# Optimization experiments

Hardware: AMD Instinct MI355X
Metric: run time of the kernel (lower is better)

Reference implementation:

```python
import jax, jax.numpy as jnp
import numpy as np

EMBED_DIM = 128
NUM_HEADS = 16
D_K = EMBED_DIM // NUM_HEADS  # must equal n_wires = 8


def setup_inputs() -> dict:
    key = jax.random.key(0)
    k1, k2 = jax.random.split(key)
    x = jax.random.normal(k1, (8, 2048, EMBED_DIM), dtype=jnp.float32)
    theta = jax.random.normal(k2, (D_K,), dtype=jnp.float32)  # trainable RX angles, one per wire
    return {"x": x, "theta": theta}


def _quantum_measure(q, theta):
    # q: [B, H, S, 8]. RX(x)RX(theta) = RX(x+theta); product state gives <Z_i> = cos(phi_i).
    # CNOT chain C(0,1)..C(6,7),C(7,0) in Heisenberg picture:
    #   <Z_0> = prod_{i=1..7} cos(phi_i);  <Z_w> = prod_{i=0..w} cos(phi_i), w>=1.
    c = jnp.cos(q + theta)                       # [B,H,S,8]
    cp = jnp.cumprod(c, axis=-1)                 # prefix products prod_{0..w}
    z0 = jnp.prod(c[..., 1:], axis=-1, keepdims=True)
    return jnp.concatenate([z0, cp[..., 1:]], axis=-1)  # [B,H,S,8]


def reference(x, theta):
    B, S, E = x.shape
    # split heads: [B,S,E] -> [B,H,S,d_k]
    q = x.reshape(B, S, NUM_HEADS, D_K).transpose(0, 2, 1, 3)
    out = _quantum_measure(q, theta)             # [B,H,S,8]
    # merge heads back: [B,S,E]
    out = out.transpose(0, 2, 1, 3).reshape(B, S, E)
    scores = jnp.einsum('bse,bte->bst', out, out) / jnp.sqrt(jnp.float32(D_K))
    attn = jax.nn.softmax(scores, axis=-1)       # dropout = identity in eval mode
    return jnp.einsum('bst,bte->bse', attn, out)
```

## Files before the change

kernel.cpp:

```cpp
#include <hip/hip_runtime.h>

#define NB 8
#define SS 2048
#define DD 128
#define SCALE2 0.5101817664764817f
#define NEGINF -3.0e38f

typedef _Float16 f16x8 __attribute__((ext_vector_type(8)));
typedef float f32x16 __attribute__((ext_vector_type(16)));
typedef unsigned short u16;
typedef u16 u16x8 __attribute__((ext_vector_type(8)));
typedef unsigned int u32;

__device__ __forceinline__ u32 pkrtz(float a, float b) {
    u32 w;
    asm("v_cvt_pkrtz_f16_f32 %0, %1, %2" : "=v"(w) : "v"(a), "v"(b));
    return w;
}

__global__ __launch_bounds__(512) void qmeasure_kernel(const float* __restrict__ x,
                                                       const float* __restrict__ theta,
                                                       u16* __restrict__ G1,
                                                       u16* __restrict__ G2) {
    __shared__ u16 olds[32][136];
    const int bid = blockIdx.x;
    const int b = bid & 7;
    const int t = bid >> 3;
    const int tid = threadIdx.x;
    const int s = tid >> 4;
    const int c = tid & 15;

    float th[8];
    *(float4*)th = *(const float4*)theta;
    *(float4*)(th + 4) = *(const float4*)(theta + 4);

    const float* xp = x + (((size_t)b * SS + t * 32 + s) * DD) + c * 8;
    float4 a = *(const float4*)xp;
    float4 a2 = *(const float4*)(xp + 4);
    float cc[8];
    cc[0] = __cosf(a.x + th[0]);  cc[1] = __cosf(a.y + th[1]);
    cc[2] = __cosf(a.z + th[2]);  cc[3] = __cosf(a.w + th[3]);
    cc[4] = __cosf(a2.x + th[4]); cc[5] = __cosf(a2.y + th[5]);
    cc[6] = __cosf(a2.z + th[6]); cc[7] = __cosf(a2.w + th[7]);
    float o[8];
    o[1] = cc[0] * cc[1];
    o[2] = o[1] * cc[2]; o[3] = o[2] * cc[3]; o[4] = o[3] * cc[4];
    o[5] = o[4] * cc[5]; o[6] = o[5] * cc[6]; o[7] = o[6] * cc[7];
    float z = cc[1] * cc[2]; z *= cc[3]; z *= cc[4]; z *= cc[5]; z *= cc[6]; z *= cc[7];
    o[0] = z;

    u16x8 w;
#pragma unroll
    for (int e = 0; e < 8; ++e) w[e] = __builtin_bit_cast(u16, (_Float16)o[e]);
    *(u16x8*)&olds[s][c * 8] = w;
    __syncthreads();

    {
        const int kc = tid >> 6, hh = (tid >> 5) & 1, r = tid & 31;
        u16x8 g;
#pragma unroll
        for (int u = 0; u < 8; ++u) g[u] = olds[r][kc * 16 + hh * 8 + u];
        *(u16x8*)(G1 + (size_t)b * (SS * DD) + ((size_t)t * 512 + tid) * 8) = g;
    }
    {
        const int lo5 = tid & 31;
        const int hh = (tid >> 5) & 1;
        const int dkc = tid >> 6;
        const int dt = dkc >> 1, kc2 = dkc & 1;
        u16x8 g;
#pragma unroll
        for (int u = 0; u < 8; ++u) g[u] = olds[kc2 * 16 + hh * 8 + u][dt * 32 + lo5];
        const int chunk = t * 512 + dkc * 64 + hh * 32 + lo5;
        *(u16x8*)(G2 + (size_t)b * (SS * DD) + (size_t)chunk * 8) = g;
    }
}

__global__ __launch_bounds__(256, 4) void qattn_kernel(const u16* __restrict__ G1g,
                                                       const u16* __restrict__ G2g,
                                                       float* __restrict__ out) {
    __shared__ float obuf[3][4][16][64];
    __shared__ float mlb[3][2][32];

    const int tid = threadIdx.x;
    const int lane = tid & 63;
    const int kq = tid >> 6;
    const int lo5 = lane & 31;
    const int hi = lane >> 5;
    const int bid = blockIdx.x;
    const int b = bid & 7;
    const int qt = bid >> 3;
    const int lane8 = lane * 8;

    const u16* G1b = G1g + (size_t)b * (SS * DD);
    const u16* G2b = G2g + (size_t)b * (SS * DD);

    f16x8 qf[8];
    {
        const u16* qp = G1b + (size_t)qt * 4096 + lane8;
#pragma unroll
        for (int kc = 0; kc < 8; ++kc) qf[kc] = *(const f16x8*)(qp + kc * 512);
    }

    f32x16 accT[4];
#pragma unroll
    for (int dt = 0; dt < 4; ++dt)
#pragma unroll
        for (int e = 0; e < 16; ++e) accT[dt][e] = 0.f;
    float m = NEGINF, l = 0.f;

    for (int it = 0; it < 16; ++it) {
        const int t = kq * 16 + it;
        const u16* kp = G1b + (size_t)t * 4096 + lane8;
        const u16* vp = G2b + (size_t)t * 4096 + lane8;

        f32x16 acc;
#pragma unroll
        for (int e = 0; e < 16; ++e) acc[e] = 0.f;
        __builtin_amdgcn_s_setprio(1);
#pragma unroll
        for (int kc = 0; kc < 8; ++kc) {
            f16x8 kf = *(const f16x8*)(kp + kc * 512);
            acc = __builtin_amdgcn_mfma_f32_32x32x16_f16(kf, qf[kc], acc, 0, 0, 0);
        }
        __builtin_amdgcn_s_setprio(0);

        float ma = fmaxf(fmaxf(acc[0], acc[1]), acc[2]);
        float mb = fmaxf(fmaxf(acc[8], acc[9]), acc[10]);
        ma = fmaxf(fmaxf(ma, acc[3]), acc[4]);
        mb = fmaxf(fmaxf(mb, acc[11]), acc[12]);
        ma = fmaxf(fmaxf(ma, acc[5]), acc[6]);
        mb = fmaxf(fmaxf(mb, acc[13]), acc[14]);
        ma = fmaxf(fmaxf(ma, acc[7]), mb);
        float tmax = fmaxf(ma, acc[15]) * SCALE2;
        tmax = fmaxf(tmax, __shfl_xor(tmax, 32));
        if (!__all(tmax <= m + 8.f)) {
            const float mnew = fmaxf(m, tmax);
            const float corr = exp2f(m - mnew);
            l *= corr;
#pragma unroll
            for (int dt = 0; dt < 4; ++dt)
#pragma unroll
                for (int e = 0; e < 16; ++e) accT[dt][e] *= corr;
            m = mnew;
        }
#pragma unroll
        for (int r = 0; r < 16; ++r) acc[r] = exp2f(acc[r] * SCALE2 - m);
        float s0 = (acc[0] + acc[1]) + (acc[2] + acc[3]);
        float s1 = (acc[4] + acc[5]) + (acc[6] + acc[7]);
        float s2 = (acc[8] + acc[9]) + (acc[10] + acc[11]);
        float s3 = (acc[12] + acc[13]) + (acc[14] + acc[15]);
        float rowsum = (s0 + s1) + (s2 + s3);
        rowsum += __shfl_xor(rowsum, 32);
        l += rowsum;

        f16x8 pa[2];
#pragma unroll
        for (int kc2 = 0; kc2 < 2; ++kc2) {
            const int r0 = kc2 * 8;
            u32 w0 = pkrtz(acc[r0 + 0], acc[r0 + 1]);
            u32 w2 = pkrtz(acc[r0 + 4], acc[r0 + 5]);
            asm("v_permlane32_swap_b32 %0, %1" : "+v"(w0), "+v"(w2));
            u32 w1 = pkrtz(acc[r0 + 2], acc[r0 + 3]);
            u32 w3 = pkrtz(acc[r0 + 6], acc[r0 + 7]);
            asm("v_permlane32_swap_b32 %0, %1" : "+v"(w1), "+v"(w3));
            union { u32 w[4]; f16x8 v; } u;
            u.w[0] = w0; u.w[1] = w1; u.w[2] = w2; u.w[3] = w3;
            pa[kc2] = u.v;
        }

        __builtin_amdgcn_s_setprio(1);
#pragma unroll
        for (int dt = 0; dt < 4; ++dt) {
            f16x8 vf0 = *(const f16x8*)(vp + (dt * 2 + 0) * 512);
            f16x8 vf1 = *(const f16x8*)(vp + (dt * 2 + 1) * 512);
            f32x16 a = accT[dt];
            a = __builtin_amdgcn_mfma_f32_32x32x16_f16(vf0, pa[0], a, 0, 0, 0);
            a = __builtin_amdgcn_mfma_f32_32x32x16_f16(vf1, pa[1], a, 0, 0, 0);
            accT[dt] = a;
        }
        __builtin_amdgcn_s_setprio(0);
    }

    if (kq > 0) {
        if (hi == 0) {
            mlb[kq - 1][0][lo5] = m;
            mlb[kq - 1][1][lo5] = l;
        }
#pragma unroll
        for (int dt = 0; dt < 4; ++dt)
#pragma unroll
            for (int r = 0; r < 16; ++r)
                obuf[kq - 1][dt][r][lane] = accT[dt][r];
    }
    __syncthreads();
    if (kq == 0) {
        const float mj0 = mlb[0][0][lo5], lj0 = mlb[0][1][lo5];
        const float mj1 = mlb[1][0][lo5], lj1 = mlb[1][1][lo5];
        const float mj2 = mlb[2][0][lo5], lj2 = mlb[2][1][lo5];
        const float ms = fmaxf(fmaxf(m, mj0), fmaxf(mj1, mj2));
        const float w0 = exp2f(m - ms), w1 = exp2f(mj0 - ms);
        const float w2 = exp2f(mj1 - ms), w3 = exp2f(mj2 - ms);
        const float linv = 1.f / (l * w0 + lj0 * w1 + lj1 * w2 + lj2 * w3);
        float* orow = out + ((size_t)b * SS + qt * 32 + lo5) * DD;
#pragma unroll
        for (int dt = 0; dt < 4; ++dt)
#pragma unroll
            for (int r = 0; r < 16; ++r) {
                const float o = accT[dt][r] * w0 + obuf[0][dt][r][lane] * w1 +
                                obuf[1][dt][r][lane] * w2 + obuf[2][dt][r][lane] * w3;
                const int drow = (r & 3) + 8 * (r >> 2) + 4 * hi;
                orow[dt * 32 + drow] = o * linv;
            }
    }
}

extern "C" void kernel_launch(void* const* d_in, const int* in_sizes, int n_in,
                              void* d_out, int out_size, void* d_ws, size_t ws_size,
                              hipStream_t stream) {
    const float* x = (const float*)d_in[0];
    const float* theta = (const float*)d_in[1];
    float* outp = (float*)d_out;
    u16* G1 = (u16*)d_ws;
    u16* G2 = G1 + (size_t)NB * SS * DD;

    qmeasure_kernel<<<512, 512, 0, stream>>>(x, theta, G1, G2);
    qattn_kernel<<<512, 256, 0, stream>>>(G1, G2, outp);
}
```

Before: 40.25 us.

## Split attention key range across eight waves per block with two-phase merge

Doubles the attention block to 512 threads so each of eight waves handles eight key tiles instead of sixteen, halving the serial loop length per wave. The cross-wave softmax merge now combines eight partial (m, l, acc) sets, staged through shared memory in two halves to limit LDS size. This trades more LDS traffic, extra barriers and a longer serial merge in wave 0 for more waves in flight and shorter per-wave dependency chains. Launch bounds of 512 threads with 4 blocks per CU may also tighten register limits.

```diff
diff --git a/kernel.cpp b/kernel.cpp
--- a/kernel.cpp
+++ b/kernel.cpp
@@ -75,11 +75,11 @@
     }
 }
 
-__global__ __launch_bounds__(256, 4) void qattn_kernel(const u16* __restrict__ G1g,
+__global__ __launch_bounds__(512, 4) void qattn_kernel(const u16* __restrict__ G1g,
                                                        const u16* __restrict__ G2g,
                                                        float* __restrict__ out) {
-    __shared__ float obuf[3][4][16][64];
-    __shared__ float mlb[3][2][32];
+    __shared__ float obuf[7][2][16][64];
+    __shared__ float mlb[7][2][32];
 
     const int tid = threadIdx.x;
     const int lane = tid & 63;
@@ -108,8 +108,8 @@
         for (int e = 0; e < 16; ++e) accT[dt][e] = 0.f;
     float m = NEGINF, l = 0.f;
 
-    for (int it = 0; it < 16; ++it) {
-        const int t = kq * 16 + it;
+    for (int it = 0; it < 8; ++it) {
+        const int t = kq * 8 + it;
         const u16* kp = G1b + (size_t)t * 4096 + lane8;
         const u16* vp = G2b + (size_t)t * 4096 + lane8;
 
@@ -187,30 +187,65 @@
             mlb[kq - 1][1][lo5] = l;
         }
 #pragma unroll
-        for (int dt = 0; dt < 4; ++dt)
+        for (int dh = 0; dh < 2; ++dh)
 #pragma unroll
             for (int r = 0; r < 16; ++r)
-                obuf[kq - 1][dt][r][lane] = accT[dt][r];
-    }
-    __syncthreads();
+                obuf[kq - 1][dh][r][lane] = accT[dh][r];
+    }
+    __syncthreads();
+    float wgt[8], linv;
     if (kq == 0) {
-        const float mj0 = mlb[0][0][lo5], lj0 = mlb[0][1][lo5];
-        const float mj1 = mlb[1][0][lo5], lj1 = mlb[1][1][lo5];
-        const float mj2 = mlb[2][0][lo5], lj2 = mlb[2][1][lo5];
-        const float ms = fmaxf(fmaxf(m, mj0), fmaxf(mj1, mj2));
-        const float w0 = exp2f(m - ms), w1 = exp2f(mj0 - ms);
-        const float w2 = exp2f(mj1 - ms), w3 = exp2f(mj2 - ms);
-        const float linv = 1.f / (l * w0 + lj0 * w1 + lj1 * w2 + lj2 * w3);
+        float mm[8], ll[8];
+        mm[0] = m; ll[0] = l;
+#pragma unroll
+        for (int j = 1; j < 8; ++j) {
+            mm[j] = mlb[j - 1][0][lo5];
+            ll[j] = mlb[j - 1][1][lo5];
+        }
+        float ms = fmaxf(fmaxf(fmaxf(mm[0], mm[1]), fmaxf(mm[2], mm[3])),
+                         fmaxf(fmaxf(mm[4], mm[5]), fmaxf(mm[6], mm[7])));
+        float den = 0.f;
+#pragma unroll
+        for (int j = 0; j < 8; ++j) {
+            wgt[j] = exp2f(mm[j] - ms);
+            den += ll[j] * wgt[j];
+        }
+        linv = 1.f / den;
         float* orow = out + ((size_t)b * SS + qt * 32 + lo5) * DD;
 #pragma unroll
-        for (int dt = 0; dt < 4; ++dt)
+        for (int dt = 0; dt < 2; ++dt)
 #pragma unroll
             for (int r = 0; r < 16; ++r) {
-                const float o = accT[dt][r] * w0 + obuf[0][dt][r][lane] * w1 +
-                                obuf[1][dt][r][lane] * w2 + obuf[2][dt][r][lane] * w3;
+                float o = accT[dt][r] * wgt[0];
+#pragma unroll
+                for (int j = 1; j < 8; ++j) o += obuf[j - 1][dt][r][lane] * wgt[j];
                 const int drow = (r & 3) + 8 * (r >> 2) + 4 * hi;
                 orow[dt * 32 + drow] = o * linv;
             }
+    }
+    __syncthreads();
+    if (kq > 0) {
+#pragma unroll
+        for (int dh = 0; dh < 2; ++dh)
+#pragma unroll
+            for (int r = 0; r < 16; ++r)
+                obuf[kq - 1][dh][r][lane] = accT[2 + dh][r];
+    }
+    __syncthreads();
+    if (kq == 0) {
+        float* orow = out + ((size_t)b * SS + qt * 32 + lo5) * DD;
+#pragma unroll
+        for (int dh = 0; dh < 2; ++dh) {
+            const int dt = 2 + dh;
+#pragma unroll
+            for (int r = 0; r < 16; ++r) {
+                float o = accT[dt][r] * wgt[0];
+#pragma unroll
+                for (int j = 1; j < 8; ++j) o += obuf[j - 1][dh][r][lane] * wgt[j];
+                const int drow = (r & 3) + 8 * (r >> 2) + 4 * hi;
+                orow[dt * 32 + drow] = o * linv;
+            }
+        }
     }
 }
 
@@ -224,5 +259,5 @@
     u16* G2 = G1 + (size_t)NB * SS * DD;
 
     qmeasure_kernel<<<512, 512, 0, stream>>>(x, theta, G1, G2);
-    qattn_kernel<<<512, 256, 0, stream>>>(G1, G2, outp);
-}
+    qattn_kernel<<<512, 512, 0, stream>>>(G1, G2, outp);
+}
```

Measured after the change: 46.39 us. +15.2%, slower.
